# Kernel optimization log

Measured on AMD Instinct MI355X. Metric: run time of the kernel, lower is better.

The kernel has to match this reference:

```python
import jax, jax.numpy as jnp
import numpy as np


def setup_inputs() -> dict:
    key = jax.random.key(0)
    k1, k2, k3, k4 = jax.random.split(key, 4)
    B, S, D = 32, 2048, 128
    queries = jax.random.normal(k1, (B, S, D), dtype=jnp.float32)
    keys = jax.random.normal(k2, (B, S, D), dtype=jnp.float32)
    values = jax.random.normal(k3, (B, S, D), dtype=jnp.float32)
    mask = jax.random.randint(k4, (B, 1, S), 0, 2, dtype=jnp.int32)
    return {"queries": queries, "keys": keys, "values": values, "mask": mask}


def reference(queries, keys, values, mask):
    # scores: [B, Sq, Sk]
    scores = jnp.einsum("bqd,bkd->bqk", queries, keys)
    pad = (mask == 0)  # broadcasts [B,1,Sk] over queries
    min_value = jnp.finfo(scores.dtype).min
    scores = jnp.where(pad, min_value, scores)
    attn = jax.nn.softmax(scores, axis=-1)
    attn = jnp.where(pad, jnp.array(0.0, attn.dtype), attn)
    return jnp.einsum("bqk,bkd->bqd", attn, values)
```

## Files before the change

kernel.cpp:

```cpp
#include <hip/hip_runtime.h>
#include <stdint.h>

#define Bb 32
#define Ss 2048
#define Dd 128
#define KVB 64
#define NIT (Ss / KVB)

typedef __attribute__((ext_vector_type(2))) float f32x2;
typedef __attribute__((ext_vector_type(4))) float f32x4;
typedef __attribute__((ext_vector_type(16))) float f32x16;
typedef __attribute__((ext_vector_type(8))) _Float16 f16x8;
typedef __attribute__((ext_vector_type(2))) __fp16 fp16x2;
typedef __attribute__((ext_vector_type(8))) unsigned short u16x8;
typedef __attribute__((ext_vector_type(4))) unsigned short u16x4;

union F16_8 { u16x8 u; uint32_t w[4]; f16x8 h; };
union F16_4 { u16x4 u; uint32_t w[2]; };

__device__ __forceinline__ uint32_t pk2(float a, float b) {
    union { fp16x2 h; uint32_t u; } v;
    v.h = __builtin_amdgcn_cvt_pkrtz(a, b);
    return v.u;
}

__global__ __launch_bounds__(256)
void attn_prep(const float* __restrict__ K, const float* __restrict__ V,
               const int* __restrict__ M,
               unsigned short* __restrict__ Kf, unsigned short* __restrict__ Vf,
               int* __restrict__ CNT) {
    __shared__ int scan_s[256];
    __shared__ unsigned short idx_l[Ss];
    __shared__ unsigned short vt[KVB * 128];

    const int x = blockIdx.x;
    const int b     = ((x & 7) << 2) | ((x >> 3) & 3);
    const int chunk = x >> 5;
    const int tid = threadIdx.x;

    const int* m = M + (size_t)b * Ss + tid * 8;
    int loc[8]; int csum = 0;
    {
        int4 a = *(const int4*)m;
        int4 c = *(const int4*)(m + 4);
        loc[0] = (a.x != 0); loc[1] = (a.y != 0); loc[2] = (a.z != 0); loc[3] = (a.w != 0);
        loc[4] = (c.x != 0); loc[5] = (c.y != 0); loc[6] = (c.z != 0); loc[7] = (c.w != 0);
#pragma unroll
        for (int j = 0; j < 8; ++j) csum += loc[j];
    }
    scan_s[tid] = csum;
    __syncthreads();
    for (int off = 1; off < 256; off <<= 1) {
        int v = scan_s[tid];
        int u = (tid >= off) ? scan_s[tid - off] : 0;
        __syncthreads();
        scan_s[tid] = v + u;
        __syncthreads();
    }
    const int count = scan_s[255];
    {
        int base = scan_s[tid] - csum;
#pragma unroll
        for (int j = 0; j < 8; ++j)
            if (loc[j]) idx_l[base++] = (unsigned short)(tid * 8 + j);
    }
    __syncthreads();
    if (chunk == 0 && tid == 0) CNT[b] = count;

    const int ntile = (count + 63) >> 6;
    if (chunk >= ntile) return;

    const int kb = chunk * 64;
    const size_t gbase = (size_t)b * Ss * Dd;
    const size_t fbase = ((size_t)b * 32 + chunk) * 8192;

#pragma unroll
    for (int j = 0; j < 4; ++j) {
        const int o  = tid + 256 * j;
        const int l  = o & 63;
        const int fn = o >> 6;
        const int ks = fn >> 1, n = fn & 1;
        const int s  = kb + n * 32 + (l & 31);
        const int d0 = ks * 16 + (l >> 5) * 8;
        F16_8 t;
        if (s < count) {
            const float* sp = K + gbase + (size_t)idx_l[s] * Dd + d0;
            f32x4 xv = *(const f32x4*)sp;
            f32x4 yv = *(const f32x4*)(sp + 4);
            t.w[0] = pk2(xv[0], xv[1]); t.w[1] = pk2(xv[2], xv[3]);
            t.w[2] = pk2(yv[0], yv[1]); t.w[3] = pk2(yv[2], yv[3]);
        } else {
            t.w[0] = 0u; t.w[1] = 0u; t.w[2] = 0u; t.w[3] = 0u;
        }
        *(u16x8*)(Kf + fbase + (size_t)o * 8) = t.u;
    }

    {
        const int rsub = tid >> 4;
        const int colh = (tid & 15) * 8;
#pragma unroll
        for (int it = 0; it < 4; ++it) {
            const int row = rsub + it * 16;
            const int s   = kb + row;
            F16_8 t;
            if (s < count) {
                const float* sp = V + gbase + (size_t)idx_l[s] * Dd + colh;
                f32x4 xv = *(const f32x4*)sp;
                f32x4 yv = *(const f32x4*)(sp + 4);
                t.w[0] = pk2(xv[0], xv[1]); t.w[1] = pk2(xv[2], xv[3]);
                t.w[2] = pk2(yv[0], yv[1]); t.w[3] = pk2(yv[2], yv[3]);
            } else {
                t.w[0] = 0u; t.w[1] = 0u; t.w[2] = 0u; t.w[3] = 0u;
            }
            *(u16x8*)&vt[row * 128 + colh] = t.u;
        }
    }
    __syncthreads();

#pragma unroll
    for (int j = 0; j < 4; ++j) {
        const int o  = tid + 256 * j;
        const int l  = o & 63;
        const int fn = o >> 6;
        const int dn = fn >> 2, ks = fn & 3;
        const int d  = dn * 32 + (l & 31);
        const int k0 = ks * 16 + (l >> 5) * 8;
        u16x8 t;
#pragma unroll
        for (int jj = 0; jj < 8; ++jj) t[jj] = vt[(k0 + jj) * 128 + d];
        *(u16x8*)(Vf + fbase + (size_t)o * 8) = t;
    }
}

__global__ __launch_bounds__(256) __attribute__((amdgpu_waves_per_eu(2, 2)))
void attn_fwd_f(const float* __restrict__ Q,
                const unsigned short* __restrict__ Kf,
                const unsigned short* __restrict__ Vf,
                const int* __restrict__ CNT,
                float* __restrict__ O) {
    __shared__ unsigned short K_lds[2][8192];
    __shared__ unsigned short V_lds[2][8192];

    const int tid = threadIdx.x;
    const int w   = tid >> 6;
    const int l   = tid & 63;
    const int q31 = l & 31;
    const int hi  = l >> 5;

    const int bid   = blockIdx.x;
    const int batch = (bid & 7) * 4 + (bid >> 7);
    const int qtile = (bid >> 3) & 15;

    const size_t qrow0 = (size_t)batch * Ss + qtile * 128 + w * 32;
    const size_t kfb   = (size_t)batch * 32 * 8192;

    const int count = CNT[batch];
    const int ntile = (count + KVB - 1) >> 6;

    auto gload = [&](int kv_t, const unsigned short* base, unsigned short (&dstb)[8192]) {
#pragma unroll
        for (int it = 0; it < 4; ++it) {
            const int ob = it * 4096 + w * 1024;
            const unsigned short* src = base + (size_t)kv_t * 8192 + (ob >> 1) + l * 8;
            void* dst = (char*)&dstb[0] + ob;
            __builtin_amdgcn_global_load_lds(
                (const __attribute__((address_space(1))) uint32_t*)src,
                (__attribute__((address_space(3))) uint32_t*)dst, 16, 0, 0);
        }
    };

    F16_8 ones;
    {
        uint32_t ow = (q31 < 8) ? 0x3C003C00u : 0u;
        ones.w[0] = ow; ones.w[1] = ow; ones.w[2] = ow; ones.w[3] = ow;
    }

    const f32x16 z16 = {0,0,0,0,0,0,0,0,0,0,0,0,0,0,0,0};
    f32x16 acco[4];
#pragma unroll
    for (int dn = 0; dn < 4; ++dn) acco[dn] = z16;
    f32x16 accl = z16;
    float mrun = -1e4f;

    const float LOG2E = 1.44269504088896340736f;
    if (ntile > 0) { gload(0, Kf + kfb, K_lds[0]); gload(0, Vf + kfb, V_lds[0]); }
    F16_8 qf[8];
#pragma unroll
    for (int ks = 0; ks < 8; ++ks) {
        const float* s = Q + (qrow0 + q31) * Dd + ks * 16 + hi * 8;
        f32x4 a = *(const f32x4*)s;
        f32x4 b = *(const f32x4*)(s + 4);
        qf[ks].w[0] = pk2(a[0] * LOG2E, a[1] * LOG2E);
        qf[ks].w[1] = pk2(a[2] * LOG2E, a[3] * LOG2E);
        qf[ks].w[2] = pk2(b[0] * LOG2E, b[1] * LOG2E);
        qf[ks].w[3] = pk2(b[2] * LOG2E, b[3] * LOG2E);
    }
    if (ntile > 0) __syncthreads();

    const int lb = l * 16;

    for (int t = 0; t < ntile; ++t) {
        const int bf = t & 1;
        const bool pf = (t + 1 < ntile);
        if (pf) {
            gload(t + 1, Kf + kfb, K_lds[bf ^ 1]);
            gload(t + 1, Vf + kfb, V_lds[bf ^ 1]);
        }

        f32x16 accs[2];
        accs[0] = z16; accs[1] = z16;
        const char* kl = (const char*)&K_lds[bf][0];
#pragma unroll
        for (int ks = 0; ks < 8; ++ks) {
#pragma unroll
            for (int n = 0; n < 2; ++n) {
                F16_8 kf;
                kf.u = *(const u16x8*)(kl + (ks * 2 + n) * 1024 + lb);
                accs[n] = __builtin_amdgcn_mfma_f32_32x32x16_f16(kf.h, qf[ks].h, accs[n], 0, 0, 0);
            }
        }

        if ((t == ntile - 1) && (count & 63)) {
            const int rem = count - t * 64;
#pragma unroll
            for (int n = 0; n < 2; ++n)
#pragma unroll
                for (int i = 0; i < 16; ++i) {
                    const int key = n * 32 + (i >> 2) * 8 + 4 * hi + (i & 3);
                    accs[n][i] = (key < rem) ? accs[n][i] : -1e30f;
                }
        }

        float mx[16];
#pragma unroll
        for (int i = 0; i < 16; ++i) mx[i] = fmaxf(accs[0][i], accs[1][i]);
#pragma unroll
        for (int s = 8; s >= 1; s >>= 1)
#pragma unroll
            for (int i = 0; i < s; ++i) mx[i] = fmaxf(mx[i], mx[i + s]);
        float pmax = fmaxf(mx[0], __shfl_xor(mx[0], 32));

        if (!__all(pmax - mrun <= 11.5409f)) {
            float mnew = fmaxf(mrun, pmax);
            float sc = __builtin_amdgcn_exp2f(mrun - mnew);
#pragma unroll
            for (int dn = 0; dn < 4; ++dn)
#pragma unroll
                for (int i = 0; i < 16; ++i) acco[dn][i] *= sc;
            accl[0] *= sc;
            mrun = mnew;
        }

#pragma unroll
        for (int n = 0; n < 2; ++n)
#pragma unroll
            for (int i = 0; i < 16; ++i) accs[n][i] = __builtin_amdgcn_exp2f(accs[n][i] - mrun);

        F16_8 pa[4];
#pragma unroll
        for (int ks = 0; ks < 4; ++ks) {
            int n  = ks >> 1;
            int b4 = (ks & 1) * 8;
            uint32_t x0 = pk2(accs[n][b4 + 0], accs[n][b4 + 1]);
            uint32_t x1 = pk2(accs[n][b4 + 2], accs[n][b4 + 3]);
            uint32_t y0 = pk2(accs[n][b4 + 4], accs[n][b4 + 5]);
            uint32_t y1 = pk2(accs[n][b4 + 6], accs[n][b4 + 7]);
            asm volatile("v_permlane32_swap_b32 %0, %1" : "+v"(x0), "+v"(y0));
            asm volatile("v_permlane32_swap_b32 %0, %1" : "+v"(x1), "+v"(y1));
            pa[ks].w[0] = x0; pa[ks].w[1] = x1; pa[ks].w[2] = y0; pa[ks].w[3] = y1;
        }

        const char* vl = (const char*)&V_lds[bf][0];
#pragma unroll
        for (int dn = 0; dn < 4; ++dn) {
#pragma unroll
            for (int ks = 0; ks < 4; ++ks) {
                F16_8 vf;
                vf.u = *(const u16x8*)(vl + (dn * 4 + ks) * 1024 + lb);
                acco[dn] = __builtin_amdgcn_mfma_f32_32x32x16_f16(vf.h, pa[ks].h, acco[dn], 0, 0, 0);
            }
        }
#pragma unroll
        for (int ks = 0; ks < 4; ++ks)
            accl = __builtin_amdgcn_mfma_f32_32x32x16_f16(ones.h, pa[ks].h, accl, 0, 0, 0);

        if (pf) __syncthreads();
    }

    float lv   = accl[0];
    float linv = lv > 0.f ? 1.0f / lv : 0.f;
    float* orow = O + (qrow0 + q31) * Dd;
#pragma unroll
    for (int dn = 0; dn < 4; ++dn)
#pragma unroll
        for (int rg = 0; rg < 4; ++rg) {
            f32x4 o;
            o[0] = acco[dn][rg * 4 + 0] * linv;
            o[1] = acco[dn][rg * 4 + 1] * linv;
            o[2] = acco[dn][rg * 4 + 2] * linv;
            o[3] = acco[dn][rg * 4 + 3] * linv;
            *(f32x4*)(orow + dn * 32 + rg * 8 + 4 * hi) = o;
        }
}

__global__ __launch_bounds__(256) __attribute__((amdgpu_waves_per_eu(2, 2)))
void attn_fwd(const float* __restrict__ Q,
              const float* __restrict__ K,
              const float* __restrict__ V,
              const int* __restrict__ M,
              float* __restrict__ O) {
    __shared__ unsigned short K_lds[KVB * 128];
    __shared__ unsigned short VT_lds[128 * 64];
    __shared__ float maskadd[KVB];

    const int tid = threadIdx.x;
    const int w   = tid >> 6;
    const int l   = tid & 63;
    const int q31 = l & 31;
    const int hi  = l >> 5;

    const int bid   = blockIdx.x;
    const int batch = (bid & 7) * 4 + (bid >> 7);
    const int qtile = (bid >> 3) & 15;

    const size_t qrow0  = (size_t)batch * Ss + qtile * 128 + w * 32;
    const size_t kvbase = (size_t)batch * Ss * Dd;
    const size_t mbase  = (size_t)batch * Ss;

    const int krow = tid >> 4;
    const int kcol = (tid & 15) << 3;
    const int vi   = tid & 15;
    const int vk   = (tid >> 4) << 2;

    f32x4 ka[4], kb[4];
    f32x2 vv[4][4];
    int mld = 0;

    auto issueK = [&](int kv) {
#pragma unroll
        for (int it = 0; it < 4; ++it) {
            const float* s = K + kvbase + (size_t)(kv + krow + it * 16) * Dd + kcol;
            ka[it] = *(const f32x4*)s;
            kb[it] = *(const f32x4*)(s + 4);
        }
        if (tid < KVB) mld = M[mbase + kv + tid];
    };
    auto writeK = [&]() {
#pragma unroll
        for (int it = 0; it < 4; ++it) {
            int row = krow + it * 16;
            F16_8 t;
            t.w[0] = pk2(ka[it][0], ka[it][1]);
            t.w[1] = pk2(ka[it][2], ka[it][3]);
            t.w[2] = pk2(kb[it][0], kb[it][1]);
            t.w[3] = pk2(kb[it][2], kb[it][3]);
            *(u16x8*)&K_lds[(row * 128 + kcol) ^ ((row & 7) << 3)] = t.u;
        }
        if (tid < KVB) maskadd[tid] = mld ? 0.f : -1e30f;
    };
    auto issueV = [&](int kv) {
#pragma unroll
        for (int j = 0; j < 4; ++j)
#pragma unroll
            for (int ko = 0; ko < 4; ++ko)
                vv[j][ko] = *(const f32x2*)(V + kvbase + (size_t)(kv + vk + ko) * Dd + 2 * vi + 32 * j);
    };
    auto writeV = [&]() {
#pragma unroll
        for (int j = 0; j < 4; ++j)
#pragma unroll
            for (int p = 0; p < 2; ++p) {
                int row = 2 * vi + p + 32 * j;
                F16_4 t;
                t.w[0] = pk2(vv[j][0][p], vv[j][1][p]);
                t.w[1] = pk2(vv[j][2][p], vv[j][3][p]);
                *(u16x4*)&VT_lds[row * 64 + (vk ^ ((row & 7) << 3))] = t.u;
            }
    };

    F16_8 ones;
    {
        uint32_t ow = (q31 < 8) ? 0x3C003C00u : 0u;
        ones.w[0] = ow; ones.w[1] = ow; ones.w[2] = ow; ones.w[3] = ow;
    }

    const f32x16 z16 = {0,0,0,0,0,0,0,0,0,0,0,0,0,0,0,0};
    f32x16 acco[4];
#pragma unroll
    for (int dn = 0; dn < 4; ++dn) acco[dn] = z16;
    f32x16 accl = z16;
    float mrun = -1e4f;

    const float LOG2E = 1.44269504088896340736f;
    issueK(0); issueV(0);
    F16_8 qf[8];
#pragma unroll
    for (int ks = 0; ks < 8; ++ks) {
        const float* s = Q + (qrow0 + q31) * Dd + ks * 16 + hi * 8;
        f32x4 a = *(const f32x4*)s;
        f32x4 b = *(const f32x4*)(s + 4);
        qf[ks].w[0] = pk2(a[0] * LOG2E, a[1] * LOG2E);
        qf[ks].w[1] = pk2(a[2] * LOG2E, a[3] * LOG2E);
        qf[ks].w[2] = pk2(b[0] * LOG2E, b[1] * LOG2E);
        qf[ks].w[3] = pk2(b[2] * LOG2E, b[3] * LOG2E);
    }
    writeK(); writeV();
    __syncthreads();

    for (int t = 0; t < NIT; ++t) {
        if (t < NIT - 1) issueK((t + 1) * KVB);

        f32x16 accs[2];
        accs[0] = z16; accs[1] = z16;
#pragma unroll
        for (int ks = 0; ks < 8; ++ks) {
#pragma unroll
            for (int n = 0; n < 2; ++n) {
                int row = n * 32 + q31;
                F16_8 kf;
                kf.u = *(const u16x8*)&K_lds[(row * 128 + ks * 16 + hi * 8) ^ ((row & 7) << 3)];
                accs[n] = __builtin_amdgcn_mfma_f32_32x32x16_f16(kf.h, qf[ks].h, accs[n], 0, 0, 0);
            }
        }

#pragma unroll
        for (int n = 0; n < 2; ++n)
#pragma unroll
            for (int blk = 0; blk < 4; ++blk) {
                f32x4 md = *(const f32x4*)&maskadd[n * 32 + blk * 8 + 4 * hi];
#pragma unroll
                for (int r = 0; r < 4; ++r) accs[n][blk * 4 + r] += md[r];
            }

        float mx[16];
#pragma unroll
        for (int i = 0; i < 16; ++i) mx[i] = fmaxf(accs[0][i], accs[1][i]);
#pragma unroll
        for (int s = 8; s >= 1; s >>= 1)
#pragma unroll
            for (int i = 0; i < s; ++i) mx[i] = fmaxf(mx[i], mx[i + s]);
        float pmax = fmaxf(mx[0], __shfl_xor(mx[0], 32));

        if (!__all(pmax - mrun <= 11.5409f)) {
            float mnew = fmaxf(mrun, pmax);
            float sc = __builtin_amdgcn_exp2f(mrun - mnew);
#pragma unroll
            for (int dn = 0; dn < 4; ++dn)
#pragma unroll
                for (int i = 0; i < 16; ++i) acco[dn][i] *= sc;
            accl[0] *= sc;
            mrun = mnew;
        }

#pragma unroll
        for (int n = 0; n < 2; ++n)
#pragma unroll
            for (int i = 0; i < 16; ++i) accs[n][i] = __builtin_amdgcn_exp2f(accs[n][i] - mrun);

        F16_8 pa[4];
#pragma unroll
        for (int ks = 0; ks < 4; ++ks) {
            int n  = ks >> 1;
            int b4 = (ks & 1) * 8;
            uint32_t x0 = pk2(accs[n][b4 + 0], accs[n][b4 + 1]);
            uint32_t x1 = pk2(accs[n][b4 + 2], accs[n][b4 + 3]);
            uint32_t y0 = pk2(accs[n][b4 + 4], accs[n][b4 + 5]);
            uint32_t y1 = pk2(accs[n][b4 + 6], accs[n][b4 + 7]);
            asm volatile("v_permlane32_swap_b32 %0, %1" : "+v"(x0), "+v"(y0));
            asm volatile("v_permlane32_swap_b32 %0, %1" : "+v"(x1), "+v"(y1));
            pa[ks].w[0] = x0; pa[ks].w[1] = x1; pa[ks].w[2] = y0; pa[ks].w[3] = y1;
        }

        __syncthreads();
        if (t < NIT - 1) { writeK(); issueV((t + 1) * KVB); }

#pragma unroll
        for (int dn = 0; dn < 4; ++dn) {
            int row = dn * 32 + q31;
#pragma unroll
            for (int ks = 0; ks < 4; ++ks) {
                F16_8 vf;
                vf.u = *(const u16x8*)&VT_lds[row * 64 + ((ks * 16 + hi * 8) ^ ((row & 7) << 3))];
                acco[dn] = __builtin_amdgcn_mfma_f32_32x32x16_f16(vf.h, pa[ks].h, acco[dn], 0, 0, 0);
            }
        }
#pragma unroll
        for (int ks = 0; ks < 4; ++ks)
            accl = __builtin_amdgcn_mfma_f32_32x32x16_f16(ones.h, pa[ks].h, accl, 0, 0, 0);

        __syncthreads();
        if (t < NIT - 1) writeV();
    }

    float lv   = accl[0];
    float linv = lv > 0.f ? 1.0f / lv : 0.f;
    float* orow = O + (qrow0 + q31) * Dd;
#pragma unroll
    for (int dn = 0; dn < 4; ++dn)
#pragma unroll
        for (int rg = 0; rg < 4; ++rg) {
            f32x4 o;
            o[0] = acco[dn][rg * 4 + 0] * linv;
            o[1] = acco[dn][rg * 4 + 1] * linv;
            o[2] = acco[dn][rg * 4 + 2] * linv;
            o[3] = acco[dn][rg * 4 + 3] * linv;
            *(f32x4*)(orow + dn * 32 + rg * 8 + 4 * hi) = o;
        }
}

extern "C" void kernel_launch(void* const* d_in, const int* in_sizes, int n_in,
                              void* d_out, int out_size, void* d_ws, size_t ws_size,
                              hipStream_t stream) {
    const float* Q = (const float*)d_in[0];
    const float* K = (const float*)d_in[1];
    const float* V = (const float*)d_in[2];
    const int*   M = (const int*)d_in[3];
    float* O = (float*)d_out;

    const size_t nF   = (size_t)Bb * 32 * 8192;
    const size_t need = nF * 2 * 2 + (size_t)Bb * 4;

    if (d_ws != nullptr && ws_size >= need) {
        unsigned short* Kf  = (unsigned short*)d_ws;
        unsigned short* Vf  = Kf + nF;
        int*            CNT = (int*)(Vf + nF);
        attn_prep<<<dim3(Bb * 32), dim3(256), 0, stream>>>(K, V, M, Kf, Vf, CNT);
        attn_fwd_f<<<dim3(Bb * (Ss / 128)), dim3(256), 0, stream>>>(Q, Kf, Vf, CNT, O);
    } else {
        attn_fwd<<<dim3(Bb * (Ss / 128)), dim3(256), 0, stream>>>(Q, K, V, M, O);
    }
}
```

Before: 65.72 us.

## Transpose V in registers and process two chunks per prep block

The prep kernel now handles two 64-key chunks per block, halving the grid, so the mask scan and index compaction run half as many times. The V transpose no longer goes through an LDS staging buffer with a barrier. Each thread gathers float2 pieces from four rows, packs them to fp16 and writes 4-element fragments directly into the fragment layout. The trade-off is fewer blocks, less parallelism and smaller, partly strided global stores.

```diff
diff --git a/kernel.cpp b/kernel.cpp
--- a/kernel.cpp
+++ b/kernel.cpp
@@ -31,11 +31,10 @@
                int* __restrict__ CNT) {
     __shared__ int scan_s[256];
     __shared__ unsigned short idx_l[Ss];
-    __shared__ unsigned short vt[KVB * 128];
 
     const int x = blockIdx.x;
-    const int b     = ((x & 7) << 2) | ((x >> 3) & 3);
-    const int chunk = x >> 5;
+    const int b      = ((x & 7) << 2) | ((x >> 3) & 3);
+    const int chunk2 = x >> 5;
     const int tid = threadIdx.x;
 
     const int* m = M + (size_t)b * Ss + tid * 8;
@@ -65,46 +64,34 @@
             if (loc[j]) idx_l[base++] = (unsigned short)(tid * 8 + j);
     }
     __syncthreads();
-    if (chunk == 0 && tid == 0) CNT[b] = count;
+    if (chunk2 == 0 && tid == 0) CNT[b] = count;
 
     const int ntile = (count + 63) >> 6;
-    if (chunk >= ntile) return;
-
-    const int kb = chunk * 64;
     const size_t gbase = (size_t)b * Ss * Dd;
-    const size_t fbase = ((size_t)b * 32 + chunk) * 8192;
-
-#pragma unroll
-    for (int j = 0; j < 4; ++j) {
-        const int o  = tid + 256 * j;
-        const int l  = o & 63;
-        const int fn = o >> 6;
-        const int ks = fn >> 1, n = fn & 1;
-        const int s  = kb + n * 32 + (l & 31);
-        const int d0 = ks * 16 + (l >> 5) * 8;
-        F16_8 t;
-        if (s < count) {
-            const float* sp = K + gbase + (size_t)idx_l[s] * Dd + d0;
-            f32x4 xv = *(const f32x4*)sp;
-            f32x4 yv = *(const f32x4*)(sp + 4);
-            t.w[0] = pk2(xv[0], xv[1]); t.w[1] = pk2(xv[2], xv[3]);
-            t.w[2] = pk2(yv[0], yv[1]); t.w[3] = pk2(yv[2], yv[3]);
-        } else {
-            t.w[0] = 0u; t.w[1] = 0u; t.w[2] = 0u; t.w[3] = 0u;
-        }
-        *(u16x8*)(Kf + fbase + (size_t)o * 8) = t.u;
-    }
-
-    {
-        const int rsub = tid >> 4;
-        const int colh = (tid & 15) * 8;
-#pragma unroll
-        for (int it = 0; it < 4; ++it) {
-            const int row = rsub + it * 16;
-            const int s   = kb + row;
+
+    const int vi = tid & 15;
+    const int vk = (tid >> 4) << 2;
+    const int vks = vk >> 4;
+    const int vhi = (vk >> 3) & 1;
+    const int ko0 = vk & 4;
+
+    for (int cc = 0; cc < 2; ++cc) {
+        const int chunk = chunk2 * 2 + cc;
+        if (chunk >= ntile) break;
+        const int kb = chunk * 64;
+        const size_t fbase = ((size_t)b * 32 + chunk) * 8192;
+
+#pragma unroll
+        for (int j = 0; j < 4; ++j) {
+            const int o  = tid + 256 * j;
+            const int l  = o & 63;
+            const int fn = o >> 6;
+            const int ks = fn >> 1, n = fn & 1;
+            const int s  = kb + n * 32 + (l & 31);
+            const int d0 = ks * 16 + (l >> 5) * 8;
             F16_8 t;
             if (s < count) {
-                const float* sp = V + gbase + (size_t)idx_l[s] * Dd + colh;
+                const float* sp = K + gbase + (size_t)idx_l[s] * Dd + d0;
                 f32x4 xv = *(const f32x4*)sp;
                 f32x4 yv = *(const f32x4*)(sp + 4);
                 t.w[0] = pk2(xv[0], xv[1]); t.w[1] = pk2(xv[2], xv[3]);
@@ -112,23 +99,32 @@
             } else {
                 t.w[0] = 0u; t.w[1] = 0u; t.w[2] = 0u; t.w[3] = 0u;
             }
-            *(u16x8*)&vt[row * 128 + colh] = t.u;
-        }
-    }
-    __syncthreads();
-
-#pragma unroll
-    for (int j = 0; j < 4; ++j) {
-        const int o  = tid + 256 * j;
-        const int l  = o & 63;
-        const int fn = o >> 6;
-        const int dn = fn >> 2, ks = fn & 3;
-        const int d  = dn * 32 + (l & 31);
-        const int k0 = ks * 16 + (l >> 5) * 8;
-        u16x8 t;
-#pragma unroll
-        for (int jj = 0; jj < 8; ++jj) t[jj] = vt[(k0 + jj) * 128 + d];
-        *(u16x8*)(Vf + fbase + (size_t)o * 8) = t;
+            *(u16x8*)(Kf + fbase + (size_t)o * 8) = t.u;
+        }
+
+        int rr[4];
+#pragma unroll
+        for (int ko = 0; ko < 4; ++ko) {
+            const int s = kb + vk + ko;
+            rr[ko] = (s < count) ? (int)idx_l[s] : 0;
+        }
+        f32x2 vv[4][4];
+#pragma unroll
+        for (int j = 0; j < 4; ++j)
+#pragma unroll
+            for (int ko = 0; ko < 4; ++ko)
+                vv[j][ko] = *(const f32x2*)(V + gbase + (size_t)rr[ko] * Dd + 2 * vi + 32 * j);
+#pragma unroll
+        for (int j = 0; j < 4; ++j)
+#pragma unroll
+            for (int p = 0; p < 2; ++p) {
+                const int l  = (2 * vi + p) + 32 * vhi;
+                const int fn = j * 4 + vks;
+                F16_4 t;
+                t.w[0] = pk2(vv[j][0][p], vv[j][1][p]);
+                t.w[1] = pk2(vv[j][2][p], vv[j][3][p]);
+                *(u16x4*)(Vf + fbase + fn * 512 + l * 8 + ko0) = t.u;
+            }
     }
 }
 
@@ -524,7 +520,7 @@
         unsigned short* Kf  = (unsigned short*)d_ws;
         unsigned short* Vf  = Kf + nF;
         int*            CNT = (int*)(Vf + nF);
-        attn_prep<<<dim3(Bb * 32), dim3(256), 0, stream>>>(K, V, M, Kf, Vf, CNT);
+        attn_prep<<<dim3(Bb * 16), dim3(256), 0, stream>>>(K, V, M, Kf, Vf, CNT);
         attn_fwd_f<<<dim3(Bb * (Ss / 128)), dim3(256), 0, stream>>>(Q, Kf, Vf, CNT, O);
     } else {
         attn_fwd<<<dim3(Bb * (Ss / 128)), dim3(256), 0, stream>>>(Q, K, V, M, O);
```

Result: no change. 67.02 us (+2.0%).
